# Kernel optimization log

Hardware: AMD Instinct MI355X
Metric: run time of the kernel (lower is better)

## Reference

```python
import jax, jax.numpy as jnp
import numpy as np
from jax import lax

BOS, EOS = 1, 2
MAX_LEN = 16
BEAM = 4
VOCAB = 32000
INF = 1e9


def _gather_beams(x, idx):
    # x: [B, K, ...] or [B, K]; idx: [B, k]
    if x.ndim == 3:
        return jnp.take_along_axis(x, idx[:, :, None], axis=1)
    return jnp.take_along_axis(x, idx, axis=1)


def setup_inputs() -> dict:
    key = jax.random.key(0)
    k1, k2, k3, k4 = jax.random.split(key, 4)
    B, S, D = 16, 128, 512
    return {
        "src_input": jax.random.randint(k1, (B, S), 0, VOCAB),
        "E_src": jax.random.normal(k2, (VOCAB, D), jnp.float32) * 0.02,
        "E_tgt": jax.random.normal(k3, (VOCAB, D), jnp.float32) * 0.02,
        "W": jax.random.normal(k4, (D, VOCAB), jnp.float32) * 0.02,
        "b": jnp.zeros((VOCAB,), jnp.float32),
    }


def _beam_search(src_input, E_src, E_tgt, W, b):
    B = src_input.shape[0]
    # tile_by_beam: repeat each batch row beam_size times
    src = jnp.repeat(src_input, BEAM, axis=0)                     # [B*BEAM, S]
    # stub encoder: embedding + masked mean pool (pad token = 0)
    enc = E_src[src]                                              # [B*BEAM, S, D]
    keep = (src != 0).astype(enc.dtype)[..., None]
    pooled = (enc * keep).sum(1) / jnp.maximum(keep.sum(1), 1.0)  # [B*BEAM, D]

    alive_seq = jnp.zeros((B, BEAM, MAX_LEN), jnp.int32).at[:, :, 0].set(BOS)
    alive_lp = jnp.full((B, BEAM), -jnp.inf, jnp.float32).at[:, 0].set(0.0)
    fin_seq = jnp.zeros((B, BEAM, MAX_LEN), jnp.int32)
    fin_scores = jnp.full((B, BEAM), -INF, jnp.float32)
    fin_flags = jnp.zeros((B, BEAM), bool)
    batch_fin = jnp.zeros((B,), bool)
    batch_idx = jnp.arange(B)[:, None]

    for t in range(MAX_LEN - 1):
        # stub decoder: last-token embedding + encoder summary -> vocab logits
        last = alive_seq[:, :, t].reshape(B * BEAM)
        logits = (E_tgt[last] + pooled) @ W + b                   # [B*BEAM, V]
        lp = jax.nn.log_softmax(logits, axis=-1).reshape(B, BEAM, VOCAB)
        log_probs = alive_lp[:, :, None] + lp                     # [B, BEAM, V]
        lpen = jnp.float32(t + 1)
        flat = (log_probs / lpen).reshape(B, BEAM * VOCAB)
        topk_scores, topk_ids = lax.top_k(flat, BEAM * 2)         # [B, 2*BEAM]
        topk_lp = topk_scores * lpen
        if t == 0:
            beam_idx = jnp.tile(jnp.arange(BEAM), (B, 2))
        else:
            beam_idx = topk_ids // VOCAB
        tok = topk_ids % VOCAB
        topk_seq = alive_seq[batch_idx, beam_idx]                 # [B, 2*BEAM, L]
        topk_seq = topk_seq.at[:, :, t + 1].set(tok.astype(jnp.int32))
        topk_fin = tok == EOS
        # alive set: penalize finished candidates
        curr = topk_scores + topk_fin.astype(jnp.float32) * -INF
        _, a_idx = lax.top_k(curr, BEAM)
        alive_seq = _gather_beams(topk_seq, a_idx)
        alive_lp = _gather_beams(topk_lp, a_idx)
        # finished set: penalize unfinished + already-finished batches
        fs = (topk_scores + (1.0 - topk_fin.astype(jnp.float32)) * -INF
              + batch_fin[:, None].astype(jnp.float32) * -INF)
        cand_seq = jnp.concatenate([fin_seq, topk_seq], axis=1)   # [B, 3*BEAM, L]
        cand_sc = jnp.concatenate([fin_scores, fs], axis=1)
        cand_fl = jnp.concatenate([fin_flags, topk_fin], axis=1)
        _, f_idx = lax.top_k(cand_sc, BEAM)
        fin_seq = _gather_beams(cand_seq, f_idx)
        fin_scores = _gather_beams(cand_sc, f_idx)
        fin_flags = _gather_beams(cand_fl, f_idx)
        # batch-finished lower-bound test
        lb_alive = alive_lp[:, 0] / lpen
        lowest_fin = jnp.min(fin_scores * fin_flags.astype(jnp.float32), axis=1)
        lowest_fin = lowest_fin + (1.0 - jnp.all(fin_flags, axis=1).astype(jnp.float32)) * -INF
        batch_fin = batch_fin | (lowest_fin >= lb_alive)
    return fin_seq, fin_scores


def reference(src_input, E_src, E_tgt, W, b):
    fin_seq, _ = _beam_search(src_input, E_src, E_tgt, W, b)
    return fin_seq[:, 0]  # one_best_output [B, MAX_LEN] int32
```

## Files before the change

### kernel.cpp

```cpp
#include <hip/hip_runtime.h>
#include <math.h>

#define BATCH 16
#define SRCLEN 128
#define DIM 512
#define VOCABSZ 32000
#define BEAM 4
#define MAXLEN 16
#define NROWS (BATCH*BEAM)
#define BOS_TOK 1
#define EOS_TOK 2
#define NEGINF 1e9f
#define CHUNKS 8
#define CHUNK 4000
#define PCH 8
#define PCL (SRCLEN/PCH)

__device__ inline unsigned long long packkey(float v, int idx) {
    unsigned int fb = __float_as_uint(v);
    fb = fb ^ ((fb >> 31) ? 0xFFFFFFFFu : 0x80000000u);
    return ((unsigned long long)fb << 32) | (unsigned long long)(0xFFFFFFFFu - (unsigned int)idx);
}
__device__ inline float unpack_val(unsigned long long k) {
    unsigned int fb = (unsigned int)(k >> 32);
    fb = fb ^ ((fb >> 31) ? 0x80000000u : 0xFFFFFFFFu);
    return __uint_as_float(fb);
}
__device__ inline int unpack_id(unsigned long long k) {
    return (int)(0xFFFFFFFFu - (unsigned int)(k & 0xFFFFFFFFu));
}
__device__ inline unsigned long long shflxor64(unsigned long long x, int mask) {
    unsigned int lo = (unsigned int)x, hi = (unsigned int)(x >> 32);
    lo = (unsigned int)__shfl_xor((int)lo, mask, 64);
    hi = (unsigned int)__shfl_xor((int)hi, mask, 64);
    return ((unsigned long long)hi << 32) | (unsigned long long)lo;
}
__device__ inline unsigned long long wavemax64(unsigned long long k) {
#pragma unroll
    for (int off = 1; off < 64; off <<= 1) {
        unsigned long long o = shflxor64(k, off);
        k = (o > k) ? o : k;
    }
    return k;
}

__global__ __launch_bounds__(512) void k_pool2(const int* __restrict__ src,
                                               const float* __restrict__ Esrc,
                                               float* __restrict__ pp, float* __restrict__ pcnt) {
    int b = blockIdx.x, c = blockIdx.y;
    int d = threadIdx.x;
    float acc = 0.f, cnt = 0.f;
#pragma unroll
    for (int s = 0; s < PCL; ++s) {
        int tok = src[b * SRCLEN + c * PCL + s];
        if (tok != 0) { acc += Esrc[(size_t)tok * DIM + d]; cnt += 1.f; }
    }
    pp[(b * PCH + c) * DIM + d] = acc;
    if (d == 0) pcnt[b * PCH + c] = cnt;
}

__global__ __launch_bounds__(512) void k_poolred(const float* __restrict__ pp,
                                                 const float* __restrict__ pcnt,
                                                 float* __restrict__ pooled) {
    int b = blockIdx.x;
    int d = threadIdx.x;
    float acc = 0.f, cnt = 0.f;
#pragma unroll
    for (int c = 0; c < PCH; ++c) { acc += pp[(b * PCH + c) * DIM + d]; cnt += pcnt[b * PCH + c]; }
    pooled[b * DIM + d] = acc / fmaxf(cnt, 1.f);
}

__global__ __launch_bounds__(1024) void k_init(int* __restrict__ alive_seq, float* __restrict__ alive_lp,
                                               int* __restrict__ fin_seq, float* __restrict__ fin_scores,
                                               int* __restrict__ fin_flags, int* __restrict__ batch_fin) {
    int tid = threadIdx.x;
    alive_seq[tid] = (tid % MAXLEN == 0) ? BOS_TOK : 0;
    fin_seq[tid] = 0;
    if (tid < NROWS) {
        alive_lp[tid] = (tid % BEAM == 0) ? 0.f : -INFINITY;
        fin_scores[tid] = -NEGINF;
        fin_flags[tid] = 0;
    }
    if (tid < BATCH) batch_fin[tid] = 0;
}

__global__ __launch_bounds__(512) void k_x(const float* __restrict__ Etgt,
                                           const float* __restrict__ pooled,
                                           const int* __restrict__ alive_seq, int t,
                                           float* __restrict__ xT) {
    int i = blockIdx.x;
    int d = threadIdx.x;
    int last = alive_seq[i * MAXLEN + t];
    float v = Etgt[(size_t)last * DIM + d] + pooled[(i >> 2) * DIM + d];
    xT[d * NROWS + i] = v;
}

template<int DLEN>
__global__ __launch_bounds__(256) void k_gemm4(const float* __restrict__ xT,
                                               const float* __restrict__ W,
                                               float* __restrict__ partial) {
    int v  = blockIdx.x * 64 + (threadIdx.x & 63);
    int rq = __builtin_amdgcn_readfirstlane(threadIdx.x >> 6);
    int r0 = rq * 16;
    int z  = blockIdx.z;
    int d0 = z * DLEN;
    float acc[16];
#pragma unroll
    for (int i = 0; i < 16; ++i) acc[i] = 0.f;
    const float* wp = W + (size_t)d0 * VOCABSZ + v;
    const float* xp = xT + (size_t)d0 * NROWS + r0;
    for (int dd = 0; dd < DLEN; dd += 4) {
        float w0 = wp[0];
        float w1 = wp[(size_t)VOCABSZ];
        float w2 = wp[(size_t)2 * VOCABSZ];
        float w3 = wp[(size_t)3 * VOCABSZ];
        wp += (size_t)4 * VOCABSZ;
        const float* x0 = xp;
        const float* x1 = xp + NROWS;
        const float* x2 = xp + 2 * NROWS;
        const float* x3 = xp + 3 * NROWS;
        xp += 4 * NROWS;
#pragma unroll
        for (int i = 0; i < 16; ++i) acc[i] = fmaf(x0[i], w0, acc[i]);
#pragma unroll
        for (int i = 0; i < 16; ++i) acc[i] = fmaf(x1[i], w1, acc[i]);
#pragma unroll
        for (int i = 0; i < 16; ++i) acc[i] = fmaf(x2[i], w2, acc[i]);
#pragma unroll
        for (int i = 0; i < 16; ++i) acc[i] = fmaf(x3[i], w3, acc[i]);
    }
    float* op = partial + (size_t)z * NROWS * VOCABSZ + (size_t)r0 * VOCABSZ + v;
#pragma unroll
    for (int i = 0; i < 16; ++i) op[(size_t)i * VOCABSZ] = acc[i];
}

template<int NZ>
__global__ __launch_bounds__(1024) void k_part(const float* __restrict__ partial,
                                               const float* __restrict__ bias,
                                               float* __restrict__ pm, float* __restrict__ ps,
                                               float* __restrict__ ptopv, int* __restrict__ ptopi) {
    int row = blockIdx.x, ch = blockIdx.y;
    int tid = threadIdx.x;
    int lane = tid & 63;
    int wv = tid >> 6;
    const size_t slab = (size_t)NROWS * VOCABSZ;
    const bool valid = tid < (CHUNK / 4);

    float vals[4] = {-INFINITY, -INFINITY, -INFINITY, -INFINITY};
    if (valid) {
        const float4* l0 = (const float4*)(partial + (size_t)row * VOCABSZ + ch * CHUNK);
        float4 q = l0[tid];
#pragma unroll
        for (int zz = 1; zz < NZ; ++zz) {
            const float4* lz = (const float4*)(partial + slab * zz + (size_t)row * VOCABSZ + ch * CHUNK);
            float4 q2 = lz[tid];
            q.x += q2.x; q.y += q2.y; q.z += q2.z; q.w += q2.w;
        }
        float4 bb = ((const float4*)(bias + ch * CHUNK))[tid];
        vals[0] = q.x + bb.x; vals[1] = q.y + bb.y; vals[2] = q.z + bb.z; vals[3] = q.w + bb.w;
    }

    float m_t = fmaxf(fmaxf(vals[0], vals[1]), fmaxf(vals[2], vals[3]));
#pragma unroll
    for (int off = 1; off < 64; off <<= 1) m_t = fmaxf(m_t, __shfl_xor(m_t, off, 64));
    __shared__ float swred[16];
    if (lane == 0) swred[wv] = m_t;
    __syncthreads();
    float m = swred[0];
#pragma unroll
    for (int w = 1; w < 16; ++w) m = fmaxf(m, swred[w]);
    __syncthreads();

    float se = 0.f;
    if (valid) {
#pragma unroll
        for (int c = 0; c < 4; ++c) se += expf(vals[c] - m);
    }
#pragma unroll
    for (int off = 1; off < 64; off <<= 1) se += __shfl_xor(se, off, 64);
    if (lane == 0) swred[wv] = se;
    __syncthreads();
    if (tid == 0) {
        float s = 0.f;
#pragma unroll
        for (int w = 0; w < 16; ++w) s += swred[w];
        pm[row * CHUNKS + ch] = m;
        ps[row * CHUNKS + ch] = s;
    }

    int gi = ch * CHUNK + tid * 4;
    unsigned long long k0 = 0ULL, k1 = 0ULL, k2 = 0ULL, k3 = 0ULL;
    if (valid) {
        k0 = packkey(vals[0], gi);
        k1 = packkey(vals[1], gi + 1);
        k2 = packkey(vals[2], gi + 2);
        k3 = packkey(vals[3], gi + 3);
    }
    {
        unsigned long long tswp;
#define CSW(a,b) if (b > a) { tswp = a; a = b; b = tswp; }
        CSW(k0,k1) CSW(k2,k3) CSW(k0,k2) CSW(k1,k3) CSW(k1,k2)
#undef CSW
    }
    __shared__ unsigned long long skey[128];
    {
        int pos = 0;
        unsigned long long wtop[8];
#pragma unroll
        for (int r = 0; r < 8; ++r) {
            unsigned long long head = (pos == 0) ? k0 : (pos == 1) ? k1 :
                                      (pos == 2) ? k2 : (pos == 3) ? k3 : 0ULL;
            unsigned long long mx = wavemax64(head);
            if (head == mx && head != 0ULL) pos++;
            wtop[r] = mx;
        }
        if (lane == 0) {
#pragma unroll
            for (int r = 0; r < 8; ++r) skey[wv * 8 + r] = wtop[r];
        }
    }
    __syncthreads();
    if (tid < 64) {
        unsigned long long a = skey[tid];
        unsigned long long b2 = skey[64 + tid];
        unsigned long long hi = (a > b2) ? a : b2;
        unsigned long long lo = (a > b2) ? b2 : a;
        float* otv = ptopv + ((size_t)row * CHUNKS + ch) * 8;
        int*   oti = ptopi + ((size_t)row * CHUNKS + ch) * 8;
        int pos = 0;
#pragma unroll
        for (int r = 0; r < 8; ++r) {
            unsigned long long head = (pos == 0) ? hi : (pos == 1) ? lo : 0ULL;
            unsigned long long mx = wavemax64(head);
            if (head == mx && head != 0ULL) pos++;
            if (tid == 0) { otv[r] = unpack_val(mx); oti[r] = unpack_id(mx); }
        }
    }
}

__global__ __launch_bounds__(64) void k_mergesel(const float* __restrict__ pm, const float* __restrict__ ps,
                                                 const float* __restrict__ ptopv, const int* __restrict__ ptopi,
                                                 int* __restrict__ alive_seq, float* __restrict__ alive_lp,
                                                 int* __restrict__ fin_seq, float* __restrict__ fin_scores,
                                                 int* __restrict__ fin_flags, int* __restrict__ batch_fin, int t) {
    int b = blockIdx.x;
    int tid = threadIdx.x;
    __shared__ int aseq_old[BEAM][MAXLEN]; __shared__ int fseq_old[BEAM][MAXLEN];
    __shared__ float s_tlp[8]; __shared__ int s_ttok[8], s_tbeam[8];
    __shared__ int s_aidx[4], s_fidx[4];
    __shared__ float s_nfsc[4]; __shared__ int s_nffl[4];
    float lpen = (float)(t + 1);

    { int k = tid >> 4, p = tid & 15;
      aseq_old[k][p] = alive_seq[(b * BEAM + k) * MAXLEN + p];
      fseq_old[k][p] = fin_seq[(b * BEAM + k) * MAXLEN + p]; }

    float rv[4]; int ri[4];
#pragma unroll
    for (int k = 0; k < 4; ++k) {
        rv[k] = ptopv[(size_t)(b * BEAM + k) * 64 + tid];
        ri[k] = ptopi[(size_t)(b * BEAM + k) * 64 + tid];
    }

    float alp[4], fsc[4]; int ffl[4];
#pragma unroll
    for (int k = 0; k < 4; ++k) {
        alp[k] = alive_lp[b * BEAM + k];
        fsc[k] = fin_scores[b * BEAM + k];
        ffl[k] = fin_flags[b * BEAM + k];
    }
    int bf_old = batch_fin[b];

    float srm[4], srl[4];
#pragma unroll
    for (int k = 0; k < 4; ++k) {
        float m = -INFINITY;
#pragma unroll
        for (int c = 0; c < CHUNKS; ++c) m = fmaxf(m, pm[(b * BEAM + k) * CHUNKS + c]);
        float s = 0.f;
#pragma unroll
        for (int c = 0; c < CHUNKS; ++c) s += ps[(b * BEAM + k) * CHUNKS + c] * expf(pm[(b * BEAM + k) * CHUNKS + c] - m);
        srm[k] = m; srl[k] = logf(s);
    }

    unsigned long long key[4];
#pragma unroll
    for (int k = 0; k < 4; ++k) {
        float sh = rv[k] - srm[k];
        float lp = sh - srl[k];
        float full = alp[k] + lp;
        float cv = full / lpen;
        key[k] = packkey(cv, k * VOCABSZ + ri[k]);
    }
    {
        unsigned long long tmp;
#define CSW(a,b) if (key[b] > key[a]) { tmp = key[a]; key[a] = key[b]; key[b] = tmp; }
        CSW(0,1) CSW(2,3) CSW(0,2) CSW(1,3) CSW(1,2)
#undef CSW
    }

    float tscore[8], tlp[8]; int ttok[8], tbeam[8], tfin[8];
    int pos = 0;
#pragma unroll
    for (int r = 0; r < 8; ++r) {
        unsigned long long head = (pos == 0) ? key[0] : (pos == 1) ? key[1] :
                                  (pos == 2) ? key[2] : (pos == 3) ? key[3] : 0ULL;
        unsigned long long mx = wavemax64(head);
        if (head == mx && head != 0ULL) pos++;
        float sc = unpack_val(mx);
        int id = unpack_id(mx);
        tscore[r] = sc;
        tlp[r] = sc * lpen;
        ttok[r] = id % VOCABSZ;
        tbeam[r] = id / VOCABSZ;
        tfin[r] = (ttok[r] == EOS_TOK) ? 1 : 0;
    }

    int aidx[4];
    {
        float curr[8];
#pragma unroll
        for (int j = 0; j < 8; ++j) curr[j] = tscore[j] + (tfin[j] ? -NEGINF : 0.0f);
        unsigned int used = 0;
#pragma unroll
        for (int r = 0; r < 4; ++r) {
            float bv = 0.f; int bj = -1;
#pragma unroll
            for (int j = 0; j < 8; ++j) {
                bool skip = (used >> j) & 1u;
                bool better = !skip && (bj < 0 || curr[j] > bv);
                if (better) { bv = curr[j]; bj = j; }
            }
            used |= 1u << bj; aidx[r] = bj;
        }
    }
    int fidx[4]; float nfsc[4]; int nffl[4];
    {
        float fscand[12]; int fflcand[12];
#pragma unroll
        for (int j = 0; j < 4; ++j) { fscand[j] = fsc[j]; fflcand[j] = ffl[j]; }
#pragma unroll
        for (int q = 0; q < 8; ++q) {
            float t1 = tscore[q] + (tfin[q] ? 0.0f : -NEGINF);
            float t2 = t1 + (bf_old ? -NEGINF : 0.0f);
            fscand[4 + q] = t2; fflcand[4 + q] = tfin[q];
        }
        unsigned int used = 0;
#pragma unroll
        for (int r = 0; r < 4; ++r) {
            float bv = 0.f; int bj = -1;
#pragma unroll
            for (int j = 0; j < 12; ++j) {
                bool skip = (used >> j) & 1u;
                bool better = !skip && (bj < 0 || fscand[j] > bv);
                if (better) { bv = fscand[j]; bj = j; }
            }
            used |= 1u << bj; fidx[r] = bj;
            nfsc[r] = bv;
        }
#pragma unroll
        for (int r = 0; r < 4; ++r) {
            int bj = fidx[r]; int fl = 0;
#pragma unroll
            for (int j = 0; j < 12; ++j) if (bj == j) fl = fflcand[j];
            nffl[r] = fl;
        }
    }

    if (tid == 0) {
#pragma unroll
        for (int r = 0; r < 8; ++r) { s_tlp[r] = tlp[r]; s_ttok[r] = ttok[r]; s_tbeam[r] = tbeam[r]; }
#pragma unroll
        for (int r = 0; r < 4; ++r) { s_aidx[r] = aidx[r]; s_fidx[r] = fidx[r]; s_nfsc[r] = nfsc[r]; s_nffl[r] = nffl[r]; }
    }
    __syncthreads();

    { int k = tid >> 4, p = tid & 15;
      int j = s_aidx[k];
      int val = (p == t + 1) ? s_ttok[j] : aseq_old[s_tbeam[j]][p];
      alive_seq[(b * BEAM + k) * MAXLEN + p] = val;
      int fi = s_fidx[k]; int fval;
      if (fi < 4) fval = fseq_old[fi][p];
      else { int q = fi - 4; fval = (p == t + 1) ? s_ttok[q] : aseq_old[s_tbeam[q]][p]; }
      fin_seq[(b * BEAM + k) * MAXLEN + p] = fval; }

    if (tid < 4) {
        alive_lp[b * BEAM + tid] = s_tlp[s_aidx[tid]];
        fin_scores[b * BEAM + tid] = s_nfsc[tid];
        fin_flags[b * BEAM + tid] = s_nffl[tid];
    }
    if (tid == 0) {
        float lb = s_tlp[s_aidx[0]] / lpen;
        float lowest = nfsc[0] * (nffl[0] ? 1.f : 0.f);
        int allf = nffl[0];
#pragma unroll
        for (int k2 = 1; k2 < 4; ++k2) {
            float pz = nfsc[k2] * (nffl[k2] ? 1.f : 0.f);
            lowest = fminf(lowest, pz);
            allf = allf && nffl[k2];
        }
        lowest = lowest + (allf ? 0.f : -NEGINF);
        batch_fin[b] = bf_old || (lowest >= lb);
    }
}

__global__ __launch_bounds__(256) void k_out(const int* __restrict__ fin_seq, float* __restrict__ out) {
    int tid = threadIdx.x;
    if (tid < BATCH * MAXLEN) {
        int b = tid / MAXLEN, p = tid % MAXLEN;
        out[tid] = (float)fin_seq[(b * BEAM + 0) * MAXLEN + p];
    }
}

extern "C" void kernel_launch(void* const* d_in, const int* in_sizes, int n_in,
                              void* d_out, int out_size, void* d_ws, size_t ws_size,
                              hipStream_t stream) {
    const int*   src  = (const int*)d_in[0];
    const float* Esrc = (const float*)d_in[1];
    const float* Etgt = (const float*)d_in[2];
    const float* W    = (const float*)d_in[3];
    const float* bias = (const float*)d_in[4];
    float* out = (float*)d_out;

    const size_t slab = (size_t)NROWS * VOCABSZ * 4;
    const bool big = ws_size >= 4 * slab + (1u << 20);
    const int NZ = big ? 4 : 1;

    char* p = (char*)d_ws;
    float* partial    = (float*)p; p += NZ * slab;
    float* pooled     = (float*)p; p += BATCH * DIM * 4;
    float* xT         = (float*)p; p += DIM * NROWS * 4;
    float* pp         = (float*)p; p += BATCH * PCH * DIM * 4;
    float* pcnt       = (float*)p; p += BATCH * PCH * 4;
    float* pm         = (float*)p; p += NROWS * CHUNKS * 4;
    float* ps         = (float*)p; p += NROWS * CHUNKS * 4;
    float* ptopv      = (float*)p; p += NROWS * CHUNKS * 8 * 4;
    int*   ptopi      = (int*)p;   p += NROWS * CHUNKS * 8 * 4;
    int*   alive_seq  = (int*)p;   p += NROWS * MAXLEN * 4;
    int*   fin_seq    = (int*)p;   p += NROWS * MAXLEN * 4;
    float* alive_lp   = (float*)p; p += NROWS * 4;
    float* fin_scores = (float*)p; p += NROWS * 4;
    int*   fin_flags  = (int*)p;   p += NROWS * 4;
    int*   batch_fin  = (int*)p;   p += BATCH * 4;

    k_pool2<<<dim3(BATCH, PCH), DIM, 0, stream>>>(src, Esrc, pp, pcnt);
    k_poolred<<<BATCH, DIM, 0, stream>>>(pp, pcnt, pooled);
    k_init<<<1, 1024, 0, stream>>>(alive_seq, alive_lp, fin_seq, fin_scores, fin_flags, batch_fin);
    for (int t = 0; t < MAXLEN - 1; ++t) {
        k_x<<<NROWS, DIM, 0, stream>>>(Etgt, pooled, alive_seq, t, xT);
        if (big) {
            k_gemm4<DIM/4><<<dim3(VOCABSZ / 64, 1, 4), 256, 0, stream>>>(xT, W, partial);
            k_part<4><<<dim3(NROWS, CHUNKS), 1024, 0, stream>>>(partial, bias, pm, ps, ptopv, ptopi);
        } else {
            k_gemm4<DIM><<<dim3(VOCABSZ / 64, 1, 1), 256, 0, stream>>>(xT, W, partial);
            k_part<1><<<dim3(NROWS, CHUNKS), 1024, 0, stream>>>(partial, bias, pm, ps, ptopv, ptopi);
        }
        k_mergesel<<<BATCH, 64, 0, stream>>>(pm, ps, ptopv, ptopi, alive_seq, alive_lp,
                                             fin_seq, fin_scores, fin_flags, batch_fin, t);
    }
    k_out<<<1, 256, 0, stream>>>(fin_seq, out);
}
```

Before: 1.122 ms.

## Replace split-K vocab GEMM with 4x4 register-tiled float4 kernel

Replaces the split-K GEMM, where each thread computed 16 rows by one vocab column, with a single-pass kernel. In the new kernel each 64-thread block computes a 4-row by 256-column tile using float4 loads of W and xT. Dropping split-K removes the extra partial slabs and the reduction over them in the softmax/top-k kernel, and the vectorised loads cut load instruction count. The cost is that the full W matrix is now read once per 4-row group, 16 times per decode step, with poor reuse because blocks sharing columns are scheduled far apart. That can greatly raise cache and memory traffic compared with the old layout, where the four waves of a block shared each W column.

Measured after the change: 1.671 ms. +49.0%, slower.

```diff
diff --git a/kernel.cpp b/kernel.cpp
--- a/kernel.cpp
+++ b/kernel.cpp
@@ -95,43 +95,47 @@
     xT[d * NROWS + i] = v;
 }
 
-template<int DLEN>
-__global__ __launch_bounds__(256) void k_gemm4(const float* __restrict__ xT,
-                                               const float* __restrict__ W,
-                                               float* __restrict__ partial) {
-    int v  = blockIdx.x * 64 + (threadIdx.x & 63);
-    int rq = __builtin_amdgcn_readfirstlane(threadIdx.x >> 6);
-    int r0 = rq * 16;
-    int z  = blockIdx.z;
-    int d0 = z * DLEN;
-    float acc[16];
-#pragma unroll
-    for (int i = 0; i < 16; ++i) acc[i] = 0.f;
-    const float* wp = W + (size_t)d0 * VOCABSZ + v;
-    const float* xp = xT + (size_t)d0 * NROWS + r0;
-    for (int dd = 0; dd < DLEN; dd += 4) {
-        float w0 = wp[0];
-        float w1 = wp[(size_t)VOCABSZ];
-        float w2 = wp[(size_t)2 * VOCABSZ];
-        float w3 = wp[(size_t)3 * VOCABSZ];
+__global__ __launch_bounds__(64) void k_gemm5(const float* __restrict__ xT,
+                                              const float* __restrict__ W,
+                                              float* __restrict__ partial) {
+    int lane = threadIdx.x;
+    int v0 = blockIdx.x * 256 + lane * 4;
+    int r0 = blockIdx.y * 4;
+    float4 a0 = {0.f,0.f,0.f,0.f}, a1 = a0, a2 = a0, a3 = a0;
+    const float* wp = W + v0;
+    const float* xp = xT + r0;
+#define STEP(xv, wv) \
+    a0.x = fmaf(xv.x, wv.x, a0.x); a0.y = fmaf(xv.x, wv.y, a0.y); \
+    a0.z = fmaf(xv.x, wv.z, a0.z); a0.w = fmaf(xv.x, wv.w, a0.w); \
+    a1.x = fmaf(xv.y, wv.x, a1.x); a1.y = fmaf(xv.y, wv.y, a1.y); \
+    a1.z = fmaf(xv.y, wv.z, a1.z); a1.w = fmaf(xv.y, wv.w, a1.w); \
+    a2.x = fmaf(xv.z, wv.x, a2.x); a2.y = fmaf(xv.z, wv.y, a2.y); \
+    a2.z = fmaf(xv.z, wv.z, a2.z); a2.w = fmaf(xv.z, wv.w, a2.w); \
+    a3.x = fmaf(xv.w, wv.x, a3.x); a3.y = fmaf(xv.w, wv.y, a3.y); \
+    a3.z = fmaf(xv.w, wv.z, a3.z); a3.w = fmaf(xv.w, wv.w, a3.w);
+#pragma unroll 2
+    for (int d = 0; d < DIM; d += 4) {
+        float4 w0 = *(const float4*)(wp);
+        float4 w1 = *(const float4*)(wp + (size_t)VOCABSZ);
+        float4 w2 = *(const float4*)(wp + (size_t)2 * VOCABSZ);
+        float4 w3 = *(const float4*)(wp + (size_t)3 * VOCABSZ);
         wp += (size_t)4 * VOCABSZ;
-        const float* x0 = xp;
-        const float* x1 = xp + NROWS;
-        const float* x2 = xp + 2 * NROWS;
-        const float* x3 = xp + 3 * NROWS;
+        float4 x0 = *(const float4*)(xp);
+        float4 x1 = *(const float4*)(xp + NROWS);
+        float4 x2 = *(const float4*)(xp + 2 * NROWS);
+        float4 x3 = *(const float4*)(xp + 3 * NROWS);
         xp += 4 * NROWS;
-#pragma unroll
-        for (int i = 0; i < 16; ++i) acc[i] = fmaf(x0[i], w0, acc[i]);
-#pragma unroll
-        for (int i = 0; i < 16; ++i) acc[i] = fmaf(x1[i], w1, acc[i]);
-#pragma unroll
-        for (int i = 0; i < 16; ++i) acc[i] = fmaf(x2[i], w2, acc[i]);
-#pragma unroll
-        for (int i = 0; i < 16; ++i) acc[i] = fmaf(x3[i], w3, acc[i]);
-    }
-    float* op = partial + (size_t)z * NROWS * VOCABSZ + (size_t)r0 * VOCABSZ + v;
-#pragma unroll
-    for (int i = 0; i < 16; ++i) op[(size_t)i * VOCABSZ] = acc[i];
+        STEP(x0, w0)
+        STEP(x1, w1)
+        STEP(x2, w2)
+        STEP(x3, w3)
+    }
+#undef STEP
+    float* op = partial + (size_t)r0 * VOCABSZ + v0;
+    *(float4*)(op) = a0;
+    *(float4*)(op + (size_t)VOCABSZ) = a1;
+    *(float4*)(op + (size_t)2 * VOCABSZ) = a2;
+    *(float4*)(op + (size_t)3 * VOCABSZ) = a3;
 }
 
 template<int NZ>
@@ -423,11 +427,9 @@
     float* out = (float*)d_out;
 
     const size_t slab = (size_t)NROWS * VOCABSZ * 4;
-    const bool big = ws_size >= 4 * slab + (1u << 20);
-    const int NZ = big ? 4 : 1;
 
     char* p = (char*)d_ws;
-    float* partial    = (float*)p; p += NZ * slab;
+    float* partial    = (float*)p; p += slab;
     float* pooled     = (float*)p; p += BATCH * DIM * 4;
     float* xT         = (float*)p; p += DIM * NROWS * 4;
     float* pp         = (float*)p; p += BATCH * PCH * DIM * 4;
@@ -448,13 +450,8 @@
     k_init<<<1, 1024, 0, stream>>>(alive_seq, alive_lp, fin_seq, fin_scores, fin_flags, batch_fin);
     for (int t = 0; t < MAXLEN - 1; ++t) {
         k_x<<<NROWS, DIM, 0, stream>>>(Etgt, pooled, alive_seq, t, xT);
-        if (big) {
-            k_gemm4<DIM/4><<<dim3(VOCABSZ / 64, 1, 4), 256, 0, stream>>>(xT, W, partial);
-            k_part<4><<<dim3(NROWS, CHUNKS), 1024, 0, stream>>>(partial, bias, pm, ps, ptopv, ptopi);
-        } else {
-            k_gemm4<DIM><<<dim3(VOCABSZ / 64, 1, 1), 256, 0, stream>>>(xT, W, partial);
-            k_part<1><<<dim3(NROWS, CHUNKS), 1024, 0, stream>>>(partial, bias, pm, ps, ptopv, ptopi);
-        }
+        k_gemm5<<<dim3(VOCABSZ / 256, NROWS / 4), 64, 0, stream>>>(xT, W, partial);
+        k_part<1><<<dim3(NROWS, CHUNKS), 1024, 0, stream>>>(partial, bias, pm, ps, ptopv, ptopi);
         k_mergesel<<<BATCH, 64, 0, stream>>>(pm, ps, ptopv, ptopi, alive_seq, alive_lp,
                                              fin_seq, fin_scores, fin_flags, batch_fin, t);
     }
```

## Register-block GEMM over 4 vocab columns and stage activations in shared memory

Applied to the files above, without the earlier changes.

The vocab-projection GEMM now has each thread compute a 16-row by 4-column tile, using float4 loads of W and float4 stores of the partial outputs. The activation slice for the block's depth split is staged in LDS first, replacing the repeated global reads of xT. The grid shrinks to VOCABSZ/256 blocks per depth split, and the small-workspace path moves from one split to two. This raises arithmetic intensity and load width, but with fewer blocks there is less parallelism, and the 64-float4 accumulator tile adds register pressure.

New measurement: 1.191 ms. 6.1% more time.

```diff
diff --git a/kernel.cpp b/kernel.cpp
--- a/kernel.cpp
+++ b/kernel.cpp
@@ -95,43 +95,64 @@
     xT[d * NROWS + i] = v;
 }
 
-template<int DLEN>
-__global__ __launch_bounds__(256) void k_gemm4(const float* __restrict__ xT,
+template<int GDLEN>
+__global__ __launch_bounds__(256) void k_gemm7(const float* __restrict__ xT,
                                                const float* __restrict__ W,
                                                float* __restrict__ partial) {
-    int v  = blockIdx.x * 64 + (threadIdx.x & 63);
-    int rq = __builtin_amdgcn_readfirstlane(threadIdx.x >> 6);
-    int r0 = rq * 16;
+    int lane = threadIdx.x & 63;
+    int wv   = threadIdx.x >> 6;
+    int v0 = blockIdx.x * 256 + lane * 4;
+    int r0 = wv * 16;
     int z  = blockIdx.z;
-    int d0 = z * DLEN;
-    float acc[16];
-#pragma unroll
-    for (int i = 0; i < 16; ++i) acc[i] = 0.f;
-    const float* wp = W + (size_t)d0 * VOCABSZ + v;
-    const float* xp = xT + (size_t)d0 * NROWS + r0;
-    for (int dd = 0; dd < DLEN; dd += 4) {
-        float w0 = wp[0];
-        float w1 = wp[(size_t)VOCABSZ];
-        float w2 = wp[(size_t)2 * VOCABSZ];
-        float w3 = wp[(size_t)3 * VOCABSZ];
-        wp += (size_t)4 * VOCABSZ;
-        const float* x0 = xp;
-        const float* x1 = xp + NROWS;
-        const float* x2 = xp + 2 * NROWS;
-        const float* x3 = xp + 3 * NROWS;
-        xp += 4 * NROWS;
-#pragma unroll
-        for (int i = 0; i < 16; ++i) acc[i] = fmaf(x0[i], w0, acc[i]);
-#pragma unroll
-        for (int i = 0; i < 16; ++i) acc[i] = fmaf(x1[i], w1, acc[i]);
-#pragma unroll
-        for (int i = 0; i < 16; ++i) acc[i] = fmaf(x2[i], w2, acc[i]);
-#pragma unroll
-        for (int i = 0; i < 16; ++i) acc[i] = fmaf(x3[i], w3, acc[i]);
-    }
-    float* op = partial + (size_t)z * NROWS * VOCABSZ + (size_t)r0 * VOCABSZ + v;
-#pragma unroll
-    for (int i = 0; i < 16; ++i) op[(size_t)i * VOCABSZ] = acc[i];
+    int d0 = z * GDLEN;
+
+    __shared__ float xs[GDLEN * NROWS];
+    {
+        const float4* xg = (const float4*)(xT + (size_t)d0 * NROWS);
+        float4* xs4 = (float4*)xs;
+#pragma unroll
+        for (int i = 0; i < (GDLEN * NROWS / 4) / 256; ++i)
+            xs4[i * 256 + threadIdx.x] = xg[i * 256 + threadIdx.x];
+    }
+    __syncthreads();
+
+    float4 acc[16];
+#pragma unroll
+    for (int i = 0; i < 16; ++i) acc[i] = make_float4(0.f, 0.f, 0.f, 0.f);
+
+    const float* wp = W + (size_t)d0 * VOCABSZ + v0;
+    const float* xp = xs + r0;
+#pragma unroll 2
+    for (int d = 0; d < GDLEN; ++d) {
+        float4 wq = *(const float4*)(wp);
+        wp += (size_t)VOCABSZ;
+#pragma unroll
+        for (int rq = 0; rq < 4; ++rq) {
+            float4 xr = *(const float4*)(xp + rq * 4);
+            acc[rq*4+0].x = fmaf(xr.x, wq.x, acc[rq*4+0].x);
+            acc[rq*4+0].y = fmaf(xr.x, wq.y, acc[rq*4+0].y);
+            acc[rq*4+0].z = fmaf(xr.x, wq.z, acc[rq*4+0].z);
+            acc[rq*4+0].w = fmaf(xr.x, wq.w, acc[rq*4+0].w);
+            acc[rq*4+1].x = fmaf(xr.y, wq.x, acc[rq*4+1].x);
+            acc[rq*4+1].y = fmaf(xr.y, wq.y, acc[rq*4+1].y);
+            acc[rq*4+1].z = fmaf(xr.y, wq.z, acc[rq*4+1].z);
+            acc[rq*4+1].w = fmaf(xr.y, wq.w, acc[rq*4+1].w);
+            acc[rq*4+2].x = fmaf(xr.z, wq.x, acc[rq*4+2].x);
+            acc[rq*4+2].y = fmaf(xr.z, wq.y, acc[rq*4+2].y);
+            acc[rq*4+2].z = fmaf(xr.z, wq.z, acc[rq*4+2].z);
+            acc[rq*4+2].w = fmaf(xr.z, wq.w, acc[rq*4+2].w);
+            acc[rq*4+3].x = fmaf(xr.w, wq.x, acc[rq*4+3].x);
+            acc[rq*4+3].y = fmaf(xr.w, wq.y, acc[rq*4+3].y);
+            acc[rq*4+3].z = fmaf(xr.w, wq.z, acc[rq*4+3].z);
+            acc[rq*4+3].w = fmaf(xr.w, wq.w, acc[rq*4+3].w);
+        }
+        xp += NROWS;
+    }
+
+    float* op = partial + (size_t)z * NROWS * VOCABSZ + (size_t)r0 * VOCABSZ + v0;
+#pragma unroll
+    for (int r = 0; r < 16; ++r)
+        *(float4*)(op + (size_t)r * VOCABSZ) = acc[r];
 }
 
 template<int NZ>
@@ -424,7 +445,7 @@
 
     const size_t slab = (size_t)NROWS * VOCABSZ * 4;
     const bool big = ws_size >= 4 * slab + (1u << 20);
-    const int NZ = big ? 4 : 1;
+    const int NZ = big ? 4 : 2;
 
     char* p = (char*)d_ws;
     float* partial    = (float*)p; p += NZ * slab;
@@ -449,11 +470,11 @@
     for (int t = 0; t < MAXLEN - 1; ++t) {
         k_x<<<NROWS, DIM, 0, stream>>>(Etgt, pooled, alive_seq, t, xT);
         if (big) {
-            k_gemm4<DIM/4><<<dim3(VOCABSZ / 64, 1, 4), 256, 0, stream>>>(xT, W, partial);
+            k_gemm7<DIM/4><<<dim3(VOCABSZ / 256, 1, 4), 256, 0, stream>>>(xT, W, partial);
             k_part<4><<<dim3(NROWS, CHUNKS), 1024, 0, stream>>>(partial, bias, pm, ps, ptopv, ptopi);
         } else {
-            k_gemm4<DIM><<<dim3(VOCABSZ / 64, 1, 1), 256, 0, stream>>>(xT, W, partial);
-            k_part<1><<<dim3(NROWS, CHUNKS), 1024, 0, stream>>>(partial, bias, pm, ps, ptopv, ptopi);
+            k_gemm7<DIM/2><<<dim3(VOCABSZ / 256, 1, 2), 256, 0, stream>>>(xT, W, partial);
+            k_part<2><<<dim3(NROWS, CHUNKS), 1024, 0, stream>>>(partial, bias, pm, ps, ptopv, ptopi);
         }
         k_mergesel<<<BATCH, 64, 0, stream>>>(pm, ps, ptopv, ptopi, alive_seq, alive_lp,
                                              fin_seq, fin_scores, fin_flags, batch_fin, t);
```
